# Kernel optimization log

Measured on AMD Instinct MI355X. Metric: run time of the kernel, lower is better.

Reference implementation:

```python
import jax, jax.numpy as jnp
import numpy as np

# Config (matches init_kwargs)
DIM = 64
HP_DIM = 32
NHEAD = 8
WS = 16  # window size
B, H, W = 4, 128, 128
NW = (H // WS) * (W // WS)  # 64 windows per image


def conv2d(x, w, b=None, padding=((1, 1), (1, 1)), groups=1):
    # x: NCHW, w: OIHW
    out = jax.lax.conv_general_dilated(
        x, w, window_strides=(1, 1), padding=padding,
        dimension_numbers=("NCHW", "OIHW", "NCHW"),
        feature_group_count=groups)
    if b is not None:
        out = out + b[None, :, None, None]
    return out


def window_partition(x, ws):
    # 'b c (h w1) (w w2) -> (b w1 w2) c h w'  with h=w=ws
    b, c, hh, ww = x.shape
    w1, w2 = hh // ws, ww // ws
    x = x.reshape(b, c, ws, w1, ws, w2)
    x = x.transpose(0, 3, 5, 1, 2, 4)  # (b, w1, w2, c, h, w)
    return x.reshape(b * w1 * w2, c, ws, ws)


def window_reverse(windows, ws, hh, ww):
    # '(b w1 w2) c h w -> b c (h w1) (w w2)'
    w1, w2 = hh // ws, ww // ws
    b = windows.shape[0] // (w1 * w2)
    c = windows.shape[1]
    x = windows.reshape(b, w1, w2, c, ws, ws)
    x = x.transpose(0, 3, 4, 1, 5, 2)  # (b, c, h, w1, w, w2)
    return x.reshape(b, c, hh, ww)


def setup_inputs() -> dict:
    key = jax.random.key(0)
    ks = jax.random.split(key, 12)
    inp = {
        "reused_attn": jax.random.normal(ks[0], (B * NW, NHEAD, WS * WS, WS * WS), jnp.float32),
        "refined_lms": jax.random.normal(ks[1], (B, DIM, H, W), jnp.float32),
        "hp_in": jax.random.normal(ks[2], (B, HP_DIM, H, W), jnp.float32),
        "ra_w1": jax.random.normal(ks[3], (NHEAD, NHEAD, 1, 3), jnp.float32) * 0.1,
        "ra_w2": jax.random.normal(ks[4], (NHEAD, NHEAD, 1, 1), jnp.float32) * 0.1,
        "ra_b2": jnp.zeros((NHEAD,), jnp.float32),
        "dw_w": jax.random.normal(ks[5], (DIM, 1, 3, 3), jnp.float32) * 0.1,
        "dw_b": jnp.zeros((DIM,), jnp.float32),
        "pw_w": jax.random.normal(ks[6], (DIM, DIM, 1, 1), jnp.float32) * 0.1,
        "pw_b": jnp.zeros((DIM,), jnp.float32),
        "fuse_w": jax.random.normal(ks[7], (DIM, DIM + HP_DIM, 3, 3), jnp.float32) * 0.05,
        "fuse_b": jnp.zeros((DIM,), jnp.float32),
    }
    return inp


def reference(reused_attn, refined_lms, hp_in, ra_w1, ra_w2, ra_b2,
              dw_w, dw_b, pw_w, pw_b, fuse_w, fuse_b):
    h, w = refined_lms.shape[-2:]

    # ReflashAttn: conv(1x3) -> conv(1x1)+bias -> ReLU -> softmax(-1)
    a = conv2d(reused_attn, ra_w1, None, padding=((0, 0), (1, 1)))
    a = conv2d(a, ra_w2, ra_b2, padding=((0, 0), (0, 0)))
    a = jax.nn.relu(a)
    attn = jax.nn.softmax(a, axis=-1)  # (Bw, nhead, M, N)

    # Windowed attention apply ('W' branch)
    x = window_partition(refined_lms, WS)  # (Bw, C, ws, ws)
    bw = x.shape[0]
    x = x.reshape(bw, NHEAD, DIM // NHEAD, WS * WS)  # b (nhead c) h w -> b nhead c (h w)
    x = jnp.einsum("bhmn,bhdm->bhdn", attn, x)
    x = x.reshape(bw, DIM, WS, WS)
    reflashed = window_reverse(x, WS, h, w)  # (B, C, H, W)

    # Residual(depthwise conv 3x3 -> ReLU -> conv 1x1) + x
    y = conv2d(reflashed, dw_w, dw_b, padding=((1, 1), (1, 1)), groups=DIM)
    y = jax.nn.relu(y)
    y = conv2d(y, pw_w, pw_b, padding=((0, 0), (0, 0)))
    res = y + reflashed

    # fuse conv + elementwise gate
    cat = jnp.concatenate([res, hp_in], axis=1)
    out = conv2d(cat, fuse_w, fuse_b, padding=((1, 1), (1, 1)))
    out = reflashed * out
    return (attn, out)
```

## Files before the change

### kernel.cpp

```cpp
#include <hip/hip_runtime.h>
#include <hip/hip_bf16.h>

#define BATCH 4
#define DIMC  64
#define HPD   32
#define NH    8
#define WSZ   16
#define HH    128
#define WW    128
#define BW    256
#define MTOK  256
#define IMG   (HH*WW)
#define ATTN_ELEMS ((size_t)BW*NH*MTOK*MTOK)
#define OUT_ELEMS  ((size_t)BATCH*DIMC*IMG)

#define WS_WC    0
#define WS_B2    192
#define WS_PW    256
#define WS_REFL  65536
#define WS_DWOUT (65536 + 4194304)
#define WS_RES   (65536 + 2*4194304)

__global__ void prep_kernel(const float* __restrict__ ra_w1,
                            const float* __restrict__ ra_w2,
                            const float* __restrict__ ra_b2,
                            const float* __restrict__ pw_w,
                            float* __restrict__ ws) {
  const int total = 192 + 8 + 4096;
  for (int i = blockIdx.x * blockDim.x + threadIdx.x; i < total;
       i += gridDim.x * blockDim.x) {
    if (i < 192) {
      int o = i / 24, r = i % 24, j = r / 3, k = r % 3;
      float acc = 0.f;
      #pragma unroll
      for (int t = 0; t < 8; ++t)
        acc += ra_w2[o * 8 + t] * ra_w1[(t * 8 + j) * 3 + k];
      ws[WS_WC + i] = acc;
    } else if (i < 200) {
      ws[WS_B2 + (i - 192)] = ra_b2[i - 192];
    } else {
      int q = i - 200;
      int o = q >> 6, c = q & 63;
      ws[WS_PW + c * 64 + o] = pw_w[q];
    }
  }
}

__global__ __launch_bounds__(256) void attn_kernel(
    const float* __restrict__ ra, const float* __restrict__ ws,
    float* __restrict__ attn_out) {
  __shared__ float A[8][258];
  __shared__ float wc[200];
  const int m = blockIdx.x;
  const int bw = blockIdx.y;
  const int t = threadIdx.x;

  const float* base = ra + (size_t)bw * 8 * 65536 + (size_t)m * 256;
  #pragma unroll
  for (int j = 0; j < 8; ++j)
    A[j][t + 1] = base[(size_t)j * 65536 + t];
  if (t < 8) { A[t][0] = 0.f; A[t][257] = 0.f; }
  if (t < 200) wc[t] = ws[t];
  __syncthreads();

  const int lane = t & 63;
  const int wave = t >> 6;
  const int o0 = wave * 2, o1 = o0 + 1;
  float acc0[4], acc1[4];
  const float b0 = wc[192 + o0], b1 = wc[192 + o1];
  #pragma unroll
  for (int q = 0; q < 4; ++q) { acc0[q] = b0; acc1[q] = b1; }

  #pragma unroll
  for (int j = 0; j < 8; ++j) {
    const float w00 = wc[(o0 * 8 + j) * 3 + 0];
    const float w01 = wc[(o0 * 8 + j) * 3 + 1];
    const float w02 = wc[(o0 * 8 + j) * 3 + 2];
    const float w10 = wc[(o1 * 8 + j) * 3 + 0];
    const float w11 = wc[(o1 * 8 + j) * 3 + 1];
    const float w12 = wc[(o1 * 8 + j) * 3 + 2];
    #pragma unroll
    for (int q = 0; q < 4; ++q) {
      const int n = lane + 64 * q;
      const float a0 = A[j][n], a1 = A[j][n + 1], a2 = A[j][n + 2];
      acc0[q] += w00 * a0 + w01 * a1 + w02 * a2;
      acc1[q] += w10 * a0 + w11 * a1 + w12 * a2;
    }
  }

  #pragma unroll
  for (int q = 0; q < 4; ++q) { acc0[q] = fmaxf(acc0[q], 0.f); acc1[q] = fmaxf(acc1[q], 0.f); }

  float* accs[2] = {acc0, acc1};
  const int os[2] = {o0, o1};
  #pragma unroll
  for (int hh = 0; hh < 2; ++hh) {
    float* a = accs[hh];
    float mx = fmaxf(fmaxf(a[0], a[1]), fmaxf(a[2], a[3]));
    #pragma unroll
    for (int s = 1; s < 64; s <<= 1) mx = fmaxf(mx, __shfl_xor(mx, s, 64));
    float e[4], sum = 0.f;
    #pragma unroll
    for (int q = 0; q < 4; ++q) { e[q] = __expf(a[q] - mx); sum += e[q]; }
    #pragma unroll
    for (int s = 1; s < 64; s <<= 1) sum += __shfl_xor(sum, s, 64);
    const float r = 1.f / sum;
    float* ob = attn_out + ((size_t)(bw * 8 + os[hh]) * 256 + m) * 256;
    #pragma unroll
    for (int q = 0; q < 4; ++q) ob[lane + 64 * q] = e[q] * r;
  }
}

__global__ __launch_bounds__(256) void apply_kernel(
    const float* __restrict__ attn, const float* __restrict__ lms,
    float* __restrict__ refl) {
  __shared__ __align__(16) float xs[256][8];
  const int bw = blockIdx.x, h = blockIdx.y;
  const int b = bw >> 6, wi = bw & 63, i1 = wi >> 3, i2 = wi & 7;
  const int t = threadIdx.x;

  {
    const int hh = t >> 4, wp = t & 15;
    const int yy = hh * 8 + i1, xx = wp * 8 + i2;
    #pragma unroll
    for (int d = 0; d < 8; ++d) {
      const int c = h * 8 + d;
      xs[t][d] = lms[(((size_t)b * 64 + c) * 128 + yy) * 128 + xx];
    }
  }
  __syncthreads();

  float acc[8] = {0, 0, 0, 0, 0, 0, 0, 0};
  const float* ab = attn + ((size_t)bw * 8 + h) * 65536 + t;
  #pragma unroll 4
  for (int mm = 0; mm < 256; ++mm) {
    const float av = ab[(size_t)mm << 8];
    const float4* xp = (const float4*)&xs[mm][0];
    const float4 x0 = xp[0], x1 = xp[1];
    acc[0] += av * x0.x; acc[1] += av * x0.y;
    acc[2] += av * x0.z; acc[3] += av * x0.w;
    acc[4] += av * x1.x; acc[5] += av * x1.y;
    acc[6] += av * x1.z; acc[7] += av * x1.w;
  }

  const int hh = t >> 4, wp = t & 15;
  const int yy = hh * 8 + i1, xx = wp * 8 + i2;
  #pragma unroll
  for (int d = 0; d < 8; ++d) {
    const int c = h * 8 + d;
    refl[(((size_t)b * 64 + c) * 128 + yy) * 128 + xx] = acc[d];
  }
}

__global__ __launch_bounds__(256) void dw_kernel(
    const float* __restrict__ refl, const float* __restrict__ dw_w,
    const float* __restrict__ dw_b, float* __restrict__ dwout) {
  const int idx = blockIdx.x * 256 + threadIdx.x;
  const int x = idx & 127, y = (idx >> 7) & 127;
  const int c = (idx >> 14) & 63, b = idx >> 20;
  const float* in = refl + ((size_t)(b * 64 + c) << 14);
  float w[9];
  #pragma unroll
  for (int k = 0; k < 9; ++k) w[k] = dw_w[c * 9 + k];
  float acc = dw_b[c];
  #pragma unroll
  for (int dy = 0; dy < 3; ++dy) {
    const int yy = y + dy - 1;
    if (yy < 0 || yy > 127) continue;
    #pragma unroll
    for (int dx = 0; dx < 3; ++dx) {
      const int xx = x + dx - 1;
      if (xx < 0 || xx > 127) continue;
      acc += w[dy * 3 + dx] * in[yy * 128 + xx];
    }
  }
  dwout[idx] = fmaxf(acc, 0.f);
}

__global__ __launch_bounds__(256) void pw_kernel(const float* __restrict__ ws,
                                                 const float* __restrict__ pwb,
                                                 float* __restrict__ res_out) {
  __shared__ __align__(16) float ds[64][64];
  __shared__ __align__(16) float wsm[64][64];
  const int tile = blockIdx.x, b = blockIdx.y;
  const int t = threadIdx.x;
  const float* dwout = ws + WS_DWOUT;
  const float* refl = ws + WS_REFL;
  const float* pwT = ws + WS_PW;

  for (int i = t; i < 4096; i += 256) ((float*)wsm)[i] = pwT[i];
  for (int i = t; i < 4096; i += 256) {
    const int c = i >> 6, p = i & 63;
    ds[c][p] = dwout[((size_t)(b * 64 + c) << 14) + tile * 64 + p];
  }
  __syncthreads();

  const int p = t & 63, qo = t >> 6;
  float acc[16];
  #pragma unroll
  for (int i = 0; i < 16; ++i) acc[i] = 0.f;
  for (int c = 0; c < 64; ++c) {
    const float v = ds[c][p];
    const float4* wrow = (const float4*)&wsm[c][0];
    #pragma unroll
    for (int i4 = 0; i4 < 4; ++i4) {
      const float4 w4 = wrow[qo * 4 + i4];
      acc[i4 * 4 + 0] += w4.x * v;
      acc[i4 * 4 + 1] += w4.y * v;
      acc[i4 * 4 + 2] += w4.z * v;
      acc[i4 * 4 + 3] += w4.w * v;
    }
  }
  #pragma unroll
  for (int i = 0; i < 16; ++i) {
    const int o = qo * 16 + i;
    const size_t idx = ((size_t)(b * 64 + o) << 14) + tile * 64 + p;
    res_out[idx] = acc[i] + pwb[o] + refl[idx];
  }
}

__global__ __launch_bounds__(256) void fuse_kernel(
    const float* __restrict__ ws, const float* __restrict__ hp,
    const float* __restrict__ fw, const float* __restrict__ fb,
    float* __restrict__ outp) {
  __shared__ float tile_s[2][324];
  const int tile = blockIdx.x;
  const int ocg = blockIdx.y;
  const int b = blockIdx.z;
  const int t = threadIdx.x;
  const int ty0 = (tile >> 3) * 16, tx0 = (tile & 7) * 16;
  const int py = t >> 4, px = t & 15;
  const int y = ty0 + py, x = tx0 + px;
  const float* res = ws + WS_RES;
  const float* refl = ws + WS_REFL;

  float acc[16];
  #pragma unroll
  for (int i = 0; i < 16; ++i) acc[i] = 0.f;

  auto load_tile = [&](int ic, int buf) {
    for (int i = t; i < 324; i += 256) {
      const int r = i / 18, cc = i % 18;
      const int gy = ty0 + r - 1, gx = tx0 + cc - 1;
      float v = 0.f;
      if (gy >= 0 && gy < 128 && gx >= 0 && gx < 128) {
        if (ic < 64)
          v = res[(((size_t)b * 64 + ic) * 128 + gy) * 128 + gx];
        else
          v = hp[(((size_t)b * 32 + (ic - 64)) * 128 + gy) * 128 + gx];
      }
      tile_s[buf][i] = v;
    }
  };

  load_tile(0, 0);
  int buf = 0;
  for (int ic = 0; ic < 96; ++ic) {
    __syncthreads();
    if (ic + 1 < 96) load_tile(ic + 1, buf ^ 1);
    float v[9];
    #pragma unroll
    for (int dy = 0; dy < 3; ++dy)
      #pragma unroll
      for (int dx = 0; dx < 3; ++dx)
        v[dy * 3 + dx] = tile_s[buf][(py + dy) * 18 + (px + dx)];
    #pragma unroll
    for (int i = 0; i < 16; ++i) {
      const float* wp = fw + ((size_t)(ocg * 16 + i) * 96 + ic) * 9;
      #pragma unroll
      for (int k = 0; k < 9; ++k) acc[i] += wp[k] * v[k];
    }
    buf ^= 1;
  }

  #pragma unroll
  for (int i = 0; i < 16; ++i) {
    const int o = ocg * 16 + i;
    const size_t idx = (((size_t)b * 64 + o) * 128 + y) * 128 + x;
    outp[idx] = refl[idx] * (acc[i] + fb[o]);
  }
}

extern "C" void kernel_launch(void* const* d_in, const int* in_sizes, int n_in,
                              void* d_out, int out_size, void* d_ws, size_t ws_size,
                              hipStream_t stream) {
  const float* reused = (const float*)d_in[0];
  const float* lms    = (const float*)d_in[1];
  const float* hp     = (const float*)d_in[2];
  const float* ra_w1  = (const float*)d_in[3];
  const float* ra_w2  = (const float*)d_in[4];
  const float* ra_b2  = (const float*)d_in[5];
  const float* dw_w   = (const float*)d_in[6];
  const float* dw_b   = (const float*)d_in[7];
  const float* pw_w   = (const float*)d_in[8];
  const float* pw_b   = (const float*)d_in[9];
  const float* fuse_w = (const float*)d_in[10];
  const float* fuse_b = (const float*)d_in[11];
  float* ws = (float*)d_ws;
  float* out = (float*)d_out;

  prep_kernel<<<17, 256, 0, stream>>>(ra_w1, ra_w2, ra_b2, pw_w, ws);
  attn_kernel<<<dim3(256, 256), 256, 0, stream>>>(reused, ws, out);
  apply_kernel<<<dim3(256, 8), 256, 0, stream>>>(out, lms, ws + WS_REFL);
  dw_kernel<<<16384, 256, 0, stream>>>(ws + WS_REFL, dw_w, dw_b, ws + WS_DWOUT);
  pw_kernel<<<dim3(256, 4), 256, 0, stream>>>(ws, pw_b, ws + WS_RES);
  fuse_kernel<<<dim3(64, 4, 4), 256, 0, stream>>>(ws, hp, fuse_w, fuse_b, out + ATTN_ELEMS);
}
```

Before: 1.340 ms.

## Fuse attention refinement, softmax and attention-apply into one kernel with split-M reduction

```diff
diff --git a/kernel.cpp b/kernel.cpp
--- a/kernel.cpp
+++ b/kernel.cpp
@@ -20,6 +20,8 @@
 #define WS_REFL  65536
 #define WS_DWOUT (65536 + 4194304)
 #define WS_RES   (65536 + 2*4194304)
+
+#define CHUNK 128
 
 __global__ void prep_kernel(const float* __restrict__ ra_w1,
                             const float* __restrict__ ra_w2,
@@ -46,110 +48,118 @@
   }
 }
 
-__global__ __launch_bounds__(256) void attn_kernel(
+__global__ __launch_bounds__(512, 4) void attn_apply_kernel(
     const float* __restrict__ ra, const float* __restrict__ ws,
-    float* __restrict__ attn_out) {
-  __shared__ float A[8][258];
-  __shared__ float wc[200];
-  const int m = blockIdx.x;
+    const float* __restrict__ lms, float* __restrict__ attn_out,
+    float* __restrict__ partial) {
+  __shared__ __align__(16) float As[2][8][256];
+  __shared__ __align__(16) float xw[CHUNK][64];
+
+  const int chunk = blockIdx.x;
   const int bw = blockIdx.y;
-  const int t = threadIdx.x;
-
-  const float* base = ra + (size_t)bw * 8 * 65536 + (size_t)m * 256;
-  #pragma unroll
-  for (int j = 0; j < 8; ++j)
-    A[j][t + 1] = base[(size_t)j * 65536 + t];
-  if (t < 8) { A[t][0] = 0.f; A[t][257] = 0.f; }
-  if (t < 200) wc[t] = ws[t];
-  __syncthreads();
-
-  const int lane = t & 63;
-  const int wave = t >> 6;
-  const int o0 = wave * 2, o1 = o0 + 1;
-  float acc0[4], acc1[4];
-  const float b0 = wc[192 + o0], b1 = wc[192 + o1];
-  #pragma unroll
-  for (int q = 0; q < 4; ++q) { acc0[q] = b0; acc1[q] = b1; }
-
-  #pragma unroll
-  for (int j = 0; j < 8; ++j) {
-    const float w00 = wc[(o0 * 8 + j) * 3 + 0];
-    const float w01 = wc[(o0 * 8 + j) * 3 + 1];
-    const float w02 = wc[(o0 * 8 + j) * 3 + 2];
-    const float w10 = wc[(o1 * 8 + j) * 3 + 0];
-    const float w11 = wc[(o1 * 8 + j) * 3 + 1];
-    const float w12 = wc[(o1 * 8 + j) * 3 + 2];
-    #pragma unroll
-    for (int q = 0; q < 4; ++q) {
-      const int n = lane + 64 * q;
-      const float a0 = A[j][n], a1 = A[j][n + 1], a2 = A[j][n + 2];
-      acc0[q] += w00 * a0 + w01 * a1 + w02 * a2;
-      acc1[q] += w10 * a0 + w11 * a1 + w12 * a2;
-    }
-  }
-
-  #pragma unroll
-  for (int q = 0; q < 4; ++q) { acc0[q] = fmaxf(acc0[q], 0.f); acc1[q] = fmaxf(acc1[q], 0.f); }
-
-  float* accs[2] = {acc0, acc1};
-  const int os[2] = {o0, o1};
-  #pragma unroll
-  for (int hh = 0; hh < 2; ++hh) {
-    float* a = accs[hh];
-    float mx = fmaxf(fmaxf(a[0], a[1]), fmaxf(a[2], a[3]));
-    #pragma unroll
-    for (int s = 1; s < 64; s <<= 1) mx = fmaxf(mx, __shfl_xor(mx, s, 64));
-    float e[4], sum = 0.f;
-    #pragma unroll
-    for (int q = 0; q < 4; ++q) { e[q] = __expf(a[q] - mx); sum += e[q]; }
-    #pragma unroll
-    for (int s = 1; s < 64; s <<= 1) sum += __shfl_xor(sum, s, 64);
-    const float r = 1.f / sum;
-    float* ob = attn_out + ((size_t)(bw * 8 + os[hh]) * 256 + m) * 256;
-    #pragma unroll
-    for (int q = 0; q < 4; ++q) ob[lane + 64 * q] = e[q] * r;
-  }
-}
-
-__global__ __launch_bounds__(256) void apply_kernel(
-    const float* __restrict__ attn, const float* __restrict__ lms,
-    float* __restrict__ refl) {
-  __shared__ __align__(16) float xs[256][8];
-  const int bw = blockIdx.x, h = blockIdx.y;
   const int b = bw >> 6, wi = bw & 63, i1 = wi >> 3, i2 = wi & 7;
   const int t = threadIdx.x;
-
-  {
-    const int hh = t >> 4, wp = t & 15;
+  const int h = t >> 6;
+  const int lane = t & 63;
+  const int c0 = lane << 2;
+
+  float wj[8][3];
+  #pragma unroll
+  for (int j = 0; j < 8; ++j)
+    #pragma unroll
+    for (int k = 0; k < 3; ++k)
+      wj[j][k] = ws[WS_WC + (h * 8 + j) * 3 + k];
+  const float bias = ws[WS_B2 + h];
+
+  for (int i = t; i < CHUNK * 64; i += 512) {
+    const int c = i & 63, mi = i >> 6;
+    const int m = chunk * CHUNK + mi;
+    const int hh = m >> 4, wp = m & 15;
     const int yy = hh * 8 + i1, xx = wp * 8 + i2;
+    xw[mi][c] = lms[(((size_t)b * 64 + c) * 128 + yy) * 128 + xx];
+  }
+
+  const float* g0 = ra + ((size_t)(bw * 8 + h) * 256 + (size_t)chunk * CHUNK) * 256;
+
+  __builtin_amdgcn_global_load_lds(
+      (const __attribute__((address_space(1))) void*)(g0 + lane * 4),
+      (__attribute__((address_space(3))) void*)&As[0][h][0], 16, 0, 0);
+  __syncthreads();
+
+  float4 acc[8];
+  #pragma unroll
+  for (int d = 0; d < 8; ++d) acc[d] = make_float4(0.f, 0.f, 0.f, 0.f);
+
+  int buf = 0;
+  for (int r = 0; r < CHUNK; ++r) {
+    if (r + 1 < CHUNK) {
+      __builtin_amdgcn_global_load_lds(
+          (const __attribute__((address_space(1))) void*)(g0 + (size_t)(r + 1) * 256 + lane * 4),
+          (__attribute__((address_space(3))) void*)&As[buf ^ 1][h][0], 16, 0, 0);
+    }
+
+    float v0 = bias, v1 = bias, v2 = bias, v3 = bias;
+    float EL = 0.f, ER = 0.f;
+    #pragma unroll
+    for (int j = 0; j < 8; ++j) {
+      const float4 a = *(const float4*)&As[buf][j][c0];
+      const float w0 = wj[j][0], w1 = wj[j][1], w2 = wj[j][2];
+      v0 += w1 * a.x + w2 * a.y;
+      v1 += w0 * a.x + w1 * a.y + w2 * a.z;
+      v2 += w0 * a.y + w1 * a.z + w2 * a.w;
+      v3 += w0 * a.z + w1 * a.w;
+      EL += w0 * a.w;
+      ER += w2 * a.x;
+    }
+    {
+      const float fromL = __shfl_up(EL, 1, 64);
+      const float fromR = __shfl_down(ER, 1, 64);
+      v0 += (lane == 0) ? 0.f : fromL;
+      v3 += (lane == 63) ? 0.f : fromR;
+    }
+
+    v0 = fmaxf(v0, 0.f); v1 = fmaxf(v1, 0.f);
+    v2 = fmaxf(v2, 0.f); v3 = fmaxf(v3, 0.f);
+    float e0 = __expf(v0), e1 = __expf(v1), e2 = __expf(v2), e3 = __expf(v3);
+    float s = (e0 + e1) + (e2 + e3);
+    #pragma unroll
+    for (int sft = 1; sft < 64; sft <<= 1) s += __shfl_xor(s, sft, 64);
+    const float rinv = 1.f / s;
+    const float p0 = e0 * rinv, p1 = e1 * rinv, p2 = e2 * rinv, p3 = e3 * rinv;
+
+    const int m = chunk * CHUNK + r;
+    *(float4*)(attn_out + ((size_t)(bw * 8 + h) * 256 + m) * 256 + c0) =
+        make_float4(p0, p1, p2, p3);
+
+    const float4 xa = *(const float4*)&xw[r][h * 8];
+    const float4 xb = *(const float4*)&xw[r][h * 8 + 4];
+    const float xv[8] = {xa.x, xa.y, xa.z, xa.w, xb.x, xb.y, xb.z, xb.w};
     #pragma unroll
     for (int d = 0; d < 8; ++d) {
-      const int c = h * 8 + d;
-      xs[t][d] = lms[(((size_t)b * 64 + c) * 128 + yy) * 128 + xx];
-    }
-  }
-  __syncthreads();
-
-  float acc[8] = {0, 0, 0, 0, 0, 0, 0, 0};
-  const float* ab = attn + ((size_t)bw * 8 + h) * 65536 + t;
-  #pragma unroll 4
-  for (int mm = 0; mm < 256; ++mm) {
-    const float av = ab[(size_t)mm << 8];
-    const float4* xp = (const float4*)&xs[mm][0];
-    const float4 x0 = xp[0], x1 = xp[1];
-    acc[0] += av * x0.x; acc[1] += av * x0.y;
-    acc[2] += av * x0.z; acc[3] += av * x0.w;
-    acc[4] += av * x1.x; acc[5] += av * x1.y;
-    acc[6] += av * x1.z; acc[7] += av * x1.w;
-  }
-
-  const int hh = t >> 4, wp = t & 15;
+      acc[d].x += p0 * xv[d]; acc[d].y += p1 * xv[d];
+      acc[d].z += p2 * xv[d]; acc[d].w += p3 * xv[d];
+    }
+
+    __syncthreads();
+    buf ^= 1;
+  }
+
+  float* pbase = partial + (size_t)chunk * OUT_ELEMS +
+                 ((size_t)(bw * 8 + h) * 8) * 256 + c0;
+  #pragma unroll
+  for (int d = 0; d < 8; ++d)
+    *(float4*)(pbase + d * 256) = acc[d];
+}
+
+__global__ __launch_bounds__(256) void reduce_kernel(
+    const float* __restrict__ partial, float* __restrict__ refl) {
+  const int idx = blockIdx.x * 256 + threadIdx.x;
+  const int n = idx & 255, d = (idx >> 8) & 7, h = (idx >> 11) & 7, bw = idx >> 14;
+  const int b = bw >> 6, wi = bw & 63, i1 = wi >> 3, i2 = wi & 7;
+  const int hh = n >> 4, wp = n & 15;
   const int yy = hh * 8 + i1, xx = wp * 8 + i2;
-  #pragma unroll
-  for (int d = 0; d < 8; ++d) {
-    const int c = h * 8 + d;
-    refl[(((size_t)b * 64 + c) * 128 + yy) * 128 + xx] = acc[d];
-  }
+  const float v = partial[idx] + partial[idx + OUT_ELEMS];
+  refl[(((size_t)b * 64 + (h * 8 + d)) * 128 + yy) * 128 + xx] = v;
 }
 
 __global__ __launch_bounds__(256) void dw_kernel(
@@ -300,9 +310,11 @@
   float* out = (float*)d_out;
 
   prep_kernel<<<17, 256, 0, stream>>>(ra_w1, ra_w2, ra_b2, pw_w, ws);
-  attn_kernel<<<dim3(256, 256), 256, 0, stream>>>(reused, ws, out);
-  apply_kernel<<<dim3(256, 8), 256, 0, stream>>>(out, lms, ws + WS_REFL);
+  attn_apply_kernel<<<dim3(2, 256), 512, 0, stream>>>(reused, ws, lms, out,
+                                                      ws + WS_DWOUT);
+  reduce_kernel<<<16384, 256, 0, stream>>>(ws + WS_DWOUT, ws + WS_REFL);
   dw_kernel<<<16384, 256, 0, stream>>>(ws + WS_REFL, dw_w, dw_b, ws + WS_DWOUT);
   pw_kernel<<<dim3(256, 4), 256, 0, stream>>>(ws, pw_b, ws + WS_RES);
-  fuse_kernel<<<dim3(64, 4, 4), 256, 0, stream>>>(ws, hp, fuse_w, fuse_b, out + ATTN_ELEMS);
-}
+  fuse_kernel<<<dim3(64, 4, 4), 256, 0, stream>>>(ws, hp, fuse_w, fuse_b,
+                                                  out + ATTN_ELEMS);
+}
```

After: 1.286 ms. 4.1% less time.
